# Kernel tuning notes

Measured on AMD Instinct MI355X. Metric: run time of the kernel, lower is better.

Reference implementation:

```python
import jax, jax.numpy as jnp
import numpy as np

B, N, C, H = 4, 2048, 768, 12
D = C // H  # 64
EPS = 1e-12


def setup_inputs() -> dict:
    key = jax.random.key(0)
    ks = jax.random.split(key, 8)
    s = 0.02
    return {
        "x": jax.random.normal(ks[0], (B, N, C), dtype=jnp.float32),
        "Wq": jax.random.normal(ks[1], (C, C), dtype=jnp.float32) * s,
        "bq": jnp.zeros((C,), dtype=jnp.float32),
        "Wkv": jax.random.normal(ks[2], (C, 2 * C), dtype=jnp.float32) * s,
        "bkv": jnp.zeros((2 * C,), dtype=jnp.float32),
        "Wproj": jax.random.normal(ks[3], (C, C), dtype=jnp.float32) * s,
        "bproj": jnp.zeros((C,), dtype=jnp.float32),
        "scale": jnp.full((1, H, 1, 1), D ** -0.5, dtype=jnp.float32),
    }


def _l2norm(t):
    # F.normalize(dim=-1): x / max(||x||_2, eps)
    n = jnp.sqrt(jnp.sum(t * t, axis=-1, keepdims=True))
    return t / jnp.maximum(n, EPS)


def reference(x, Wq, bq, Wkv, bkv, Wproj, bproj, scale):
    b, n, c = x.shape
    q = (x @ Wq + bq).reshape(b, n, H, D).transpose(0, 2, 1, 3)        # [B,H,N,D]
    kv = (x @ Wkv + bkv).reshape(b, n, 2, H, D).transpose(2, 0, 3, 1, 4)
    k, v = kv[0], kv[1]                                                # [B,H,N,D]
    q = _l2norm(q)
    k = _l2norm(k)
    attn = jnp.einsum("bhqd,bhkd->bhqk", q, k) * scale                 # [B,H,N,N]
    attn = jax.nn.softmax(attn, axis=-1)
    out = jnp.einsum("bhqk,bhkd->bhqd", attn, v)                       # [B,H,N,D]
    out = out.transpose(0, 2, 1, 3).reshape(b, n, c)
    return out @ Wproj + bproj
```

## Files before the change

### kernel.cpp

```cpp
#include <hip/hip_runtime.h>
#include <hip/hip_bf16.h>
#include <math.h>


typedef short bf16x8 __attribute__((ext_vector_type(8)));
typedef float f32x4 __attribute__((ext_vector_type(4)));
typedef float f32x16 __attribute__((ext_vector_type(16)));

static __device__ __forceinline__ unsigned short f2bf(float f) {
    unsigned int u = __float_as_uint(f);
    unsigned int r = u + 0x7fff + ((u >> 16) & 1);
    return (unsigned short)(r >> 16);
}
static __device__ __forceinline__ unsigned int pack2(float a, float b) {
    return (unsigned int)f2bf(a) | ((unsigned int)f2bf(b) << 16);
}
static __device__ __forceinline__ unsigned int cvtpk(float a, float b) {
    unsigned int r;
    asm("v_cvt_pk_bf16_f32 %0, %1, %2" : "=v"(r) : "v"(a), "v"(b));
    return r;
}
static __device__ __forceinline__ void gl_lds16(const void* g, void* l) {
    __builtin_amdgcn_global_load_lds(
        (const __attribute__((address_space(1))) unsigned int*)g,
        (__attribute__((address_space(3))) unsigned int*)l, 16, 0, 0);
}

__global__ __launch_bounds__(256) void convx_kernel(
    const float* __restrict__ in, unsigned short* __restrict__ out)
{
    size_t i = ((size_t)blockIdx.x * 256 + threadIdx.x) * 8;
    float4 a = *(const float4*)&in[i];
    float4 b = *(const float4*)&in[i + 4];
    uint4 o = make_uint4(pack2(a.x, a.y), pack2(a.z, a.w), pack2(b.x, b.y), pack2(b.z, b.w));
    *(uint4*)&out[i] = o;
}

__global__ __launch_bounds__(256) void convT_kernel(
    const float* __restrict__ Wq, const float* __restrict__ Wkv, const float* __restrict__ Wp,
    unsigned short* __restrict__ WqkvT, unsigned short* __restrict__ WprjT)
{
    __shared__ char tb[8192];
    const int bx = blockIdx.x, k0 = blockIdx.y * 64;
    const float* src; int ld; int cbase; unsigned short* out; int c0;
    if (bx < 36) {
        c0 = bx * 64; out = WqkvT;
        if (c0 < 768) { src = Wq;  ld = 768;  cbase = c0; }
        else          { src = Wkv; ld = 1536; cbase = c0 - 768; }
    } else {
        c0 = (bx - 36) * 64; out = WprjT; src = Wp; ld = 768; cbase = c0;
    }
    const int t = threadIdx.x;
    const int kl = t >> 2, cq = (t & 3) * 16;
    #pragma unroll
    for (int jj = 0; jj < 4; ++jj) {
        float4 v = *(const float4*)&src[(size_t)(k0 + kl) * ld + cbase + cq + jj * 4];
        float vv[4] = {v.x, v.y, v.z, v.w};
        #pragma unroll
        for (int je = 0; je < 4; ++je) {
            int c = cq + jj * 4 + je;
            *(unsigned short*)(tb + c * 128 + ((kl * 2) ^ ((c & 7) << 4))) = f2bf(vv[je]);
        }
    }
    __syncthreads();
    const int cl = t >> 2, u2 = (t & 3) * 2;
    uint4 r0 = *(const uint4*)(tb + cl * 128 + ((u2 ^ (cl & 7)) << 4));
    uint4 r1 = *(const uint4*)(tb + cl * 128 + (((u2 + 1) ^ (cl & 7)) << 4));
    size_t ob = (size_t)(c0 + cl) * 768 + k0 + (t & 3) * 16;
    *(uint4*)&out[ob] = r0;
    *(uint4*)&out[ob + 8] = r1;
}

__global__ __launch_bounds__(256) void qkv_gemm_kernel(
    const unsigned short* __restrict__ xb, const unsigned short* __restrict__ WT,
    const float* __restrict__ bq, const float* __restrict__ bkv,
    const float* __restrict__ scale,
    unsigned short* __restrict__ Qb, unsigned short* __restrict__ Kb,
    unsigned short* __restrict__ Vtb)
{
    __shared__ char lds[32768] __attribute__((aligned(16)));

    const int ct = blockIdx.x;
    const int row0 = blockIdx.y * 128;
    const int tid = threadIdx.x;
    const int w = tid >> 6, l = tid & 63;
    const int g = l >> 4, ln = l & 15;
    const int wr = w >> 1, wc = w & 1;
    const int col0 = ct * 128;

    const int srow = (w & 1) * 64 + (l >> 3);
    const int su = ((l & 7) ^ (l >> 3)) * 16;
    const char* s = (w < 2)
        ? (const char*)xb + (size_t)(row0 + srow) * 1536 + su
        : (const char*)WT + (size_t)(col0 + srow) * 1536 + su;
    char* dbase = lds + ((w >= 2) ? 16384 : 0) + (w & 1) * 8192;

    f32x4 acc[4][4];
    #pragma unroll
    for (int m = 0; m < 4; ++m)
        #pragma unroll
        for (int n = 0; n < 4; ++n) acc[m][n] = (f32x4){0.f, 0.f, 0.f, 0.f};

    const int arow = (wr * 64 + ln) * 128;
    const int brow = 16384 + (wc * 64 + ln) * 128;
    const int x0 = ((0 + g) ^ (ln & 7)) * 16;
    const int x1 = ((4 + g) ^ (ln & 7)) * 16;

    for (int ks = 0; ks < 12; ++ks) {
        __syncthreads();
        #pragma unroll
        for (int j = 0; j < 8; ++j)
            gl_lds16(s + (size_t)j * 8 * 1536, dbase + j * 1024);
        s += 128;
        __syncthreads();
        #pragma unroll
        for (int kc = 0; kc < 2; ++kc) {
            const int xo = kc ? x1 : x0;
            bf16x8 af[4], bfr[4];
            #pragma unroll
            for (int m = 0; m < 4; ++m) af[m] = *(const bf16x8*)(lds + arow + m * 2048 + xo);
            #pragma unroll
            for (int n = 0; n < 4; ++n) bfr[n] = *(const bf16x8*)(lds + brow + n * 2048 + xo);
            #pragma unroll
            for (int m = 0; m < 4; ++m)
                #pragma unroll
                for (int n = 0; n < 4; ++n)
                    acc[m][n] = __builtin_amdgcn_mfma_f32_16x16x32_bf16(af[m], bfr[n], acc[m][n], 0, 0, 0);
        }
    }

    const int co = col0 + wc * 64 + ln;
    float bv[4];
    #pragma unroll
    for (int n = 0; n < 4; ++n) {
        int c = co + n * 16;
        bv[n] = (c < 768) ? bq[c] : bkv[c - 768];
    }
    const int region = ct / 6;
    const int h = (ct % 6) * 2 + wc;

    if (region < 2) {
        unsigned short* dst = (region == 0) ? Qb : Kb;
        const float post = (region == 0) ? scale[0] * 1.4426950408889634f : 1.0f;
        #pragma unroll
        for (int m = 0; m < 4; ++m) {
            #pragma unroll
            for (int n = 0; n < 4; ++n)
                #pragma unroll
                for (int r = 0; r < 4; ++r) acc[m][n][r] += bv[n];
            #pragma unroll
            for (int r = 0; r < 4; ++r) {
                float ss = 0.f;
                #pragma unroll
                for (int n = 0; n < 4; ++n) ss += acc[m][n][r] * acc[m][n][r];
                ss += __shfl_xor(ss, 1); ss += __shfl_xor(ss, 2);
                ss += __shfl_xor(ss, 4); ss += __shfl_xor(ss, 8);
                float inv = post / fmaxf(sqrtf(ss), 1e-12f);
                int t = row0 + wr * 64 + m * 16 + g * 4 + r;
                int b = t >> 11, nt = t & 2047;
                size_t base = ((size_t)(b * 12 + h) * 2048 + nt) * 64 + ln;
                #pragma unroll
                for (int n = 0; n < 4; ++n)
                    dst[base + n * 16] = f2bf(acc[m][n][r] * inv);
            }
        }
    } else {
        char* tb = lds + w * 8192;
        __syncthreads();
        #pragma unroll
        for (int m = 0; m < 4; ++m)
            #pragma unroll
            for (int n = 0; n < 4; ++n)
                #pragma unroll
                for (int r = 0; r < 4; ++r) {
                    int d = n * 16 + ln;
                    int tok = m * 16 + g * 4 + r;
                    *(unsigned short*)(tb + d * 128 + ((tok * 2) ^ ((d & 7) << 4))) =
                        f2bf(acc[m][n][r] + bv[n]);
                }
        __syncthreads();
        const int t0 = row0 + wr * 64;
        const int b = t0 >> 11, n0 = t0 & 2047;
        #pragma unroll
        for (int i = 0; i < 8; ++i) {
            int d = i * 8 + (l >> 3);
            uint4 v = *(const uint4*)(tb + d * 128 + (((l & 7) ^ (d & 7)) << 4));
            *(uint4*)&Vtb[((size_t)(b * 12 + h) * 64 + d) * 2048 + n0 + (l & 7) * 8] = v;
        }
    }
}

__global__ __launch_bounds__(256, 3) void attn_kernel(
    const unsigned short* __restrict__ Qg, const unsigned short* __restrict__ Kg,
    const unsigned short* __restrict__ Vtg,
    unsigned short* __restrict__ O)
{
    __shared__ char lds[32768] __attribute__((aligned(16)));

    const int bid = blockIdx.y * 16 + blockIdx.x;
    const int swzb = (bid & 7) * 96 + (bid >> 3);
    const int bh = swzb >> 4;
    const int q0 = (swzb & 15) * 128;

    const int tid = threadIdx.x;
    const int w  = tid >> 6;
    const int l  = tid & 63;
    const int lo = l & 31;
    const int hi = l >> 5;

    const int srow = w * 16 + (l >> 3);
    const int su   = ((l & 7) ^ (l >> 3)) * 16;
    const char* kS = (const char*)Kg  + ((size_t)bh * 2048 + srow) * 128 + su;
    const char* vS = (const char*)Vtg + ((size_t)bh * 64   + srow) * 4096 + su;
    char* kD = lds + w * 2048;
    char* vD = lds + 16384 + w * 2048;

    bf16x8 qf[4];
    {
        const unsigned short* qp = Qg + ((size_t)bh * 2048 + q0 + w * 32 + lo) * 64 + hi * 8;
        qf[0] = *(const bf16x8*)(qp);
        qf[1] = *(const bf16x8*)(qp + 16);
        qf[2] = *(const bf16x8*)(qp + 32);
        qf[3] = *(const bf16x8*)(qp + 48);
    }

    const int swz = (lo & 7) << 4;
    const int rowb = lo * 128;
    int coff[4];
    #pragma unroll
    for (int c = 0; c < 4; ++c) coff[c] = (c * 32 + hi * 16) ^ swz;

    f32x16 oacc0, oacc1;
    #pragma unroll
    for (int r = 0; r < 16; ++r) { oacc0[r] = 0.f; oacc1[r] = 0.f; }
    float rs = 0.f;

    const f32x16 zero16 = {0.f,0.f,0.f,0.f,0.f,0.f,0.f,0.f,0.f,0.f,0.f,0.f,0.f,0.f,0.f,0.f};

    auto compute = [&](const int OFF) {
        const char* Kb = lds + OFF;
        const char* Vb = lds + 16384 + OFF;

        f32x16 s0, s1;
        __builtin_amdgcn_s_setprio(1);
        s0 = __builtin_amdgcn_mfma_f32_32x32x16_bf16(*(const bf16x8*)(Kb + rowb + coff[0]), qf[0], zero16, 0, 0, 0);
        s0 = __builtin_amdgcn_mfma_f32_32x32x16_bf16(*(const bf16x8*)(Kb + rowb + coff[1]), qf[1], s0, 0, 0, 0);
        s0 = __builtin_amdgcn_mfma_f32_32x32x16_bf16(*(const bf16x8*)(Kb + rowb + coff[2]), qf[2], s0, 0, 0, 0);
        s0 = __builtin_amdgcn_mfma_f32_32x32x16_bf16(*(const bf16x8*)(Kb + rowb + coff[3]), qf[3], s0, 0, 0, 0);
        s1 = __builtin_amdgcn_mfma_f32_32x32x16_bf16(*(const bf16x8*)(Kb + 4096 + rowb + coff[0]), qf[0], zero16, 0, 0, 0);
        s1 = __builtin_amdgcn_mfma_f32_32x32x16_bf16(*(const bf16x8*)(Kb + 4096 + rowb + coff[1]), qf[1], s1, 0, 0, 0);
        s1 = __builtin_amdgcn_mfma_f32_32x32x16_bf16(*(const bf16x8*)(Kb + 4096 + rowb + coff[2]), qf[2], s1, 0, 0, 0);
        s1 = __builtin_amdgcn_mfma_f32_32x32x16_bf16(*(const bf16x8*)(Kb + 4096 + rowb + coff[3]), qf[3], s1, 0, 0, 0);
        __builtin_amdgcn_s_setprio(0);

        #pragma unroll
        for (int r = 0; r < 16; ++r) s0[r] = __builtin_amdgcn_exp2f(s0[r]);
        #pragma unroll
        for (int r = 0; r < 16; ++r) s1[r] = __builtin_amdgcn_exp2f(s1[r]);
        float t0 = 0.f, t1 = 0.f;
        #pragma unroll
        for (int r = 0; r < 16; ++r) { t0 += s0[r]; t1 += s1[r]; }
        rs += t0 + t1;

        #pragma unroll
        for (int kb = 0; kb < 2; ++kb) {
            const f32x16 ec = kb ? s1 : s0;
            #pragma unroll
            for (int ksb = 0; ksb < 2; ++ksb) {
                const int ks = kb * 2 + ksb;
                const int rqA = ksb * 2, rqB = rqA + 1;
                unsigned int uA0 = cvtpk(ec[rqA * 4 + 0], ec[rqA * 4 + 1]);
                unsigned int uA1 = cvtpk(ec[rqA * 4 + 2], ec[rqA * 4 + 3]);
                unsigned int uB0 = cvtpk(ec[rqB * 4 + 0], ec[rqB * 4 + 1]);
                unsigned int uB1 = cvtpk(ec[rqB * 4 + 2], ec[rqB * 4 + 3]);
                asm("v_permlane32_swap_b32 %0, %1" : "+v"(uA0), "+v"(uB0));
                asm("v_permlane32_swap_b32 %0, %1" : "+v"(uA1), "+v"(uB1));
                unsigned int fw[4] = {uA0, uA1, uB0, uB1};
                bf16x8 pa;
                __builtin_memcpy(&pa, fw, 16);
                __builtin_amdgcn_s_setprio(1);
                bf16x8 v0 = *(const bf16x8*)(Vb + rowb + coff[ks]);
                bf16x8 v1 = *(const bf16x8*)(Vb + 4096 + rowb + coff[ks]);
                oacc0 = __builtin_amdgcn_mfma_f32_32x32x16_bf16(pa, v0, oacc0, 0, 0, 0);
                oacc1 = __builtin_amdgcn_mfma_f32_32x32x16_bf16(pa, v1, oacc1, 0, 0, 0);
                __builtin_amdgcn_s_setprio(0);
            }
        }
    };

    gl_lds16(kS, kD);          gl_lds16(kS + 1024, kD + 1024);
    gl_lds16(vS, vD);          gl_lds16(vS + 32768, vD + 1024);
    kS += 8192; vS += 128;
    __syncthreads();

    #pragma unroll 1
    for (int it = 0; it < 16; ++it) {
        gl_lds16(kS, kD + 8192);          gl_lds16(kS + 1024, kD + 9216);
        gl_lds16(vS, vD + 8192);          gl_lds16(vS + 32768, vD + 9216);
        kS += 8192; vS += 128;
        compute(0);
        __syncthreads();
        if (it < 15) {
            gl_lds16(kS, kD);          gl_lds16(kS + 1024, kD + 1024);
            gl_lds16(vS, vD);          gl_lds16(vS + 32768, vD + 1024);
            kS += 8192; vS += 128;
        }
        compute(8192);
        __syncthreads();
    }

    float rsv = rs;
    rsv += __shfl_xor(rsv, 32);
    const int b = bh / 12, h = bh % 12;
    #pragma unroll
    for (int r = 0; r < 16; ++r) {
        const int qr = (r & 3) + 8 * (r >> 2) + 4 * hi;
        float inv = 1.0f / __shfl(rsv, qr);
        size_t base = ((size_t)(b * 2048 + q0 + w * 32 + qr)) * 768 + h * 64 + lo;
        O[base]      = f2bf(oacc0[r] * inv);
        O[base + 32] = f2bf(oacc1[r] * inv);
    }
}

__global__ __launch_bounds__(256) void proj_gemm_kernel(
    const unsigned short* __restrict__ Ob, const unsigned short* __restrict__ WT,
    const float* __restrict__ bp, float* __restrict__ out)
{
    __shared__ char lds[32768] __attribute__((aligned(16)));

    const int row0 = blockIdx.y * 128;
    const int col0 = blockIdx.x * 128;
    const int tid = threadIdx.x;
    const int w = tid >> 6, l = tid & 63;
    const int g = l >> 4, ln = l & 15;
    const int wr = w >> 1, wc = w & 1;

    const int srow = (w & 1) * 64 + (l >> 3);
    const int su = ((l & 7) ^ (l >> 3)) * 16;
    const char* s = (w < 2)
        ? (const char*)Ob + (size_t)(row0 + srow) * 1536 + su
        : (const char*)WT + (size_t)(col0 + srow) * 1536 + su;
    char* dbase = lds + ((w >= 2) ? 16384 : 0) + (w & 1) * 8192;

    f32x4 acc[4][4];
    #pragma unroll
    for (int m = 0; m < 4; ++m)
        #pragma unroll
        for (int n = 0; n < 4; ++n) acc[m][n] = (f32x4){0.f, 0.f, 0.f, 0.f};

    const int arow = (wr * 64 + ln) * 128;
    const int brow = 16384 + (wc * 64 + ln) * 128;
    const int x0 = ((0 + g) ^ (ln & 7)) * 16;
    const int x1 = ((4 + g) ^ (ln & 7)) * 16;

    for (int ks = 0; ks < 12; ++ks) {
        __syncthreads();
        #pragma unroll
        for (int j = 0; j < 8; ++j)
            gl_lds16(s + (size_t)j * 8 * 1536, dbase + j * 1024);
        s += 128;
        __syncthreads();
        #pragma unroll
        for (int kc = 0; kc < 2; ++kc) {
            const int xo = kc ? x1 : x0;
            bf16x8 af[4], bfr[4];
            #pragma unroll
            for (int m = 0; m < 4; ++m) af[m] = *(const bf16x8*)(lds + arow + m * 2048 + xo);
            #pragma unroll
            for (int n = 0; n < 4; ++n) bfr[n] = *(const bf16x8*)(lds + brow + n * 2048 + xo);
            #pragma unroll
            for (int m = 0; m < 4; ++m)
                #pragma unroll
                for (int n = 0; n < 4; ++n)
                    acc[m][n] = __builtin_amdgcn_mfma_f32_16x16x32_bf16(af[m], bfr[n], acc[m][n], 0, 0, 0);
        }
    }

    const int co = col0 + wc * 64 + ln;
    float bv[4];
    #pragma unroll
    for (int n = 0; n < 4; ++n) bv[n] = bp[co + n * 16];
    #pragma unroll
    for (int m = 0; m < 4; ++m)
        #pragma unroll
        for (int r = 0; r < 4; ++r) {
            int t = row0 + wr * 64 + m * 16 + g * 4 + r;
            #pragma unroll
            for (int n = 0; n < 4; ++n)
                out[(size_t)t * 768 + co + n * 16] = acc[m][n][r] + bv[n];
        }
}

extern "C" void kernel_launch(void* const* d_in, const int* in_sizes, int n_in,
                              void* d_out, int out_size, void* d_ws, size_t ws_size,
                              hipStream_t stream) {
    const float* x     = (const float*)d_in[0];
    const float* Wq    = (const float*)d_in[1];
    const float* bq    = (const float*)d_in[2];
    const float* Wkv   = (const float*)d_in[3];
    const float* bkv   = (const float*)d_in[4];
    const float* Wp    = (const float*)d_in[5];
    const float* bp    = (const float*)d_in[6];
    const float* scale = (const float*)d_in[7];
    float* out = (float*)d_out;

    unsigned short* ws = (unsigned short*)d_ws;
    const size_t SZ = (size_t)4 * 12 * 2048 * 64;
    unsigned short* xbw   = ws;
    unsigned short* WqkvT = xbw + SZ;
    unsigned short* WprjT = WqkvT + (size_t)2304 * 768;
    unsigned short* Qw    = WprjT + (size_t)768 * 768;
    unsigned short* Kw    = Qw + SZ;
    unsigned short* Vtw   = Kw + SZ;
    unsigned short* Ow    = Vtw + SZ;

    convx_kernel<<<3072, 256, 0, stream>>>(x, xbw);
    convT_kernel<<<dim3(48, 12), 256, 0, stream>>>(Wq, Wkv, Wp, WqkvT, WprjT);
    qkv_gemm_kernel<<<dim3(18, 64), 256, 0, stream>>>(xbw, WqkvT, bq, bkv, scale, Qw, Kw, Vtw);
    attn_kernel<<<dim3(16, 48), 256, 0, stream>>>(Qw, Kw, Vtw, Ow);
    proj_gemm_kernel<<<dim3(6, 64), 256, 0, stream>>>(Ow, WprjT, bp, out);
}
```

Before: 143.2 us.

## Load V directly from global into registers instead of staging through LDS

The attention kernel stops staging V tiles in shared memory. Each lane now loads its own V fragments from global memory into registers right before the compute step that uses them, and LDS shrinks to hold only the double-buffered K tiles. This is meant to cut LDS traffic and footprint, which could allow more resident blocks. In exchange, V data shared across the four waves is fetched redundantly from global/L2, and global load latency is only partly hidden because each load is issued just ahead of its use.

After: 184.2 us. +28.6%, slower.

```diff
diff --git a/kernel.cpp b/kernel.cpp
--- a/kernel.cpp
+++ b/kernel.cpp
@@ -195,7 +195,7 @@
     const unsigned short* __restrict__ Vtg,
     unsigned short* __restrict__ O)
 {
-    __shared__ char lds[32768] __attribute__((aligned(16)));
+    __shared__ char lds[16384] __attribute__((aligned(16)));
 
     const int bid = blockIdx.y * 16 + blockIdx.x;
     const int swzb = (bid & 7) * 96 + (bid >> 3);
@@ -210,10 +210,11 @@
 
     const int srow = w * 16 + (l >> 3);
     const int su   = ((l & 7) ^ (l >> 3)) * 16;
-    const char* kS = (const char*)Kg  + ((size_t)bh * 2048 + srow) * 128 + su;
-    const char* vS = (const char*)Vtg + ((size_t)bh * 64   + srow) * 4096 + su;
+    const char* kS = (const char*)Kg + ((size_t)bh * 2048 + srow) * 128 + su;
     char* kD = lds + w * 2048;
-    char* vD = lds + 16384 + w * 2048;
+
+    const char* vB0 = (const char*)Vtg + ((size_t)(bh * 64 + lo) * 2048) * 2 + hi * 16;
+    const char* vB1 = vB0 + (size_t)32 * 4096;
 
     bf16x8 qf[4];
     {
@@ -237,9 +238,19 @@
 
     const f32x16 zero16 = {0.f,0.f,0.f,0.f,0.f,0.f,0.f,0.f,0.f,0.f,0.f,0.f,0.f,0.f,0.f,0.f};
 
+    bf16x8 vr[8];
+
+    auto issueV = [&]() {
+        #pragma unroll
+        for (int ks = 0; ks < 4; ++ks) {
+            vr[ks * 2]     = *(const bf16x8*)(vB0 + ks * 32);
+            vr[ks * 2 + 1] = *(const bf16x8*)(vB1 + ks * 32);
+        }
+        vB0 += 128; vB1 += 128;
+    };
+
     auto compute = [&](const int OFF) {
         const char* Kb = lds + OFF;
-        const char* Vb = lds + 16384 + OFF;
 
         f32x16 s0, s1;
         __builtin_amdgcn_s_setprio(1);
@@ -279,31 +290,28 @@
                 bf16x8 pa;
                 __builtin_memcpy(&pa, fw, 16);
                 __builtin_amdgcn_s_setprio(1);
-                bf16x8 v0 = *(const bf16x8*)(Vb + rowb + coff[ks]);
-                bf16x8 v1 = *(const bf16x8*)(Vb + 4096 + rowb + coff[ks]);
-                oacc0 = __builtin_amdgcn_mfma_f32_32x32x16_bf16(pa, v0, oacc0, 0, 0, 0);
-                oacc1 = __builtin_amdgcn_mfma_f32_32x32x16_bf16(pa, v1, oacc1, 0, 0, 0);
+                oacc0 = __builtin_amdgcn_mfma_f32_32x32x16_bf16(pa, vr[ks * 2],     oacc0, 0, 0, 0);
+                oacc1 = __builtin_amdgcn_mfma_f32_32x32x16_bf16(pa, vr[ks * 2 + 1], oacc1, 0, 0, 0);
                 __builtin_amdgcn_s_setprio(0);
             }
         }
     };
 
-    gl_lds16(kS, kD);          gl_lds16(kS + 1024, kD + 1024);
-    gl_lds16(vS, vD);          gl_lds16(vS + 32768, vD + 1024);
-    kS += 8192; vS += 128;
+    gl_lds16(kS, kD); gl_lds16(kS + 1024, kD + 1024);
+    kS += 8192;
     __syncthreads();
 
     #pragma unroll 1
     for (int it = 0; it < 16; ++it) {
-        gl_lds16(kS, kD + 8192);          gl_lds16(kS + 1024, kD + 9216);
-        gl_lds16(vS, vD + 8192);          gl_lds16(vS + 32768, vD + 9216);
-        kS += 8192; vS += 128;
+        issueV();
+        gl_lds16(kS, kD + 8192); gl_lds16(kS + 1024, kD + 9216);
+        kS += 8192;
         compute(0);
         __syncthreads();
+        issueV();
         if (it < 15) {
-            gl_lds16(kS, kD);          gl_lds16(kS + 1024, kD + 1024);
-            gl_lds16(vS, vD);          gl_lds16(vS + 32768, vD + 1024);
-            kS += 8192; vS += 128;
+            gl_lds16(kS, kD); gl_lds16(kS + 1024, kD + 1024);
+            kS += 8192;
         }
         compute(8192);
         __syncthreads();
```
